# Performance work log

Measured on AMD Instinct MI355X. Metric: run time of the kernel, lower is better.

## Reference

```python
import jax, jax.numpy as jnp
import numpy as np

NUM_HEADS = 16
NEG = -1e9


def setup_inputs() -> dict:
    key = jax.random.key(0)
    ks = jax.random.split(key, 16)
    B, Sq, Skv, E = 4, 4096, 4096, 1024
    scale = 1.0 / np.sqrt(E)
    inp = {
        "q": jax.random.normal(ks[0], (B, Sq, E), jnp.float32),
        "k": jax.random.normal(ks[1], (B, Skv, E), jnp.float32),
        "v": jax.random.normal(ks[2], (B, Skv, E), jnp.float32),
        "q_padding_mask": jax.random.randint(ks[3], (B, Sq, 1), 0, 2).astype(bool),
        "key_padding_mask": jax.random.randint(ks[4], (B, Skv, 1), 0, 2).astype(bool),
        "Wq": jax.random.normal(ks[5], (E, E), jnp.float32) * scale,
        "bq": jnp.zeros((E,), jnp.float32),
        "Wk": jax.random.normal(ks[6], (E, E), jnp.float32) * scale,
        "bk": jnp.zeros((E,), jnp.float32),
        "Wv": jax.random.normal(ks[7], (E, E), jnp.float32) * scale,
        "bv": jnp.zeros((E,), jnp.float32),
        "Wp": jax.random.normal(ks[8], (E, E), jnp.float32) * scale,
        "bp": jnp.zeros((E,), jnp.float32),
    }
    return inp


def _split_heads(x, H):
    B, S, E = x.shape
    return x.reshape(B, S, H, E // H).transpose(0, 2, 1, 3)  # (B,H,S,D)


def reference(q, k, v, q_padding_mask, key_padding_mask, Wq, bq, Wk, bk, Wv, bv, Wp, bp):
    B, Sq, E = q.shape
    H = NUM_HEADS
    # padding: q*mask + ~mask*(-1e9) == where(mask, q, -1e9)
    q = jnp.where(q_padding_mask, q, NEG)
    k = jnp.where(key_padding_mask, k, NEG)
    v = v * key_padding_mask
    # projections (torch nn.Linear: x @ W.T + b)
    qh = _split_heads(q @ Wq.T + bq, H)  # (B,H,Sq,D)
    kh = _split_heads(k @ Wk.T + bk, H)  # (B,H,Skv,D)
    vh = _split_heads(v @ Wv.T + bv, H)  # (B,H,Skv,D)
    qh = jax.nn.softmax(qh, axis=-1)
    kh = jax.nn.softmax(kh, axis=-1)
    k_cumsum = kh.sum(axis=-2, keepdims=True)              # (B,H,1,D)
    a_t = 1.0 / (qh * k_cumsum).sum(axis=-1, keepdims=True)  # (B,H,Sq,1)
    context = jnp.einsum("bhsd,bhse->bhde", kh, vh)        # (B,H,D,D)
    out = jnp.einsum("bhqd,bhde->bhqe", qh, context) * a_t + qh
    out = out.transpose(0, 2, 1, 3).reshape(B, Sq, E)
    out = out @ Wp.T + bp
    return out * q_padding_mask
```

## Files before the change

### kernel.cpp

```cpp
#include <hip/hip_runtime.h>
#include <hip/hip_bf16.h>
#include <stdint.h>


typedef __bf16 bf16_t;
typedef __bf16 v8bf __attribute__((ext_vector_type(8)));
typedef __bf16 v4bf __attribute__((ext_vector_type(4)));
typedef float  v4f  __attribute__((ext_vector_type(4)));

#define NSPLIT 16

__device__ __forceinline__ void gl_lds16(const void* g, void* l) {
  __builtin_amdgcn_global_load_lds((const __attribute__((address_space(1))) void*)g,
                                   (__attribute__((address_space(3))) void*)l,
                                   16, 0, 0);
}

__global__ __launch_bounds__(256) void convert_w(
    const float* __restrict__ W0, const float* __restrict__ W1,
    const float* __restrict__ W2, const float* __restrict__ W3,
    bf16_t* __restrict__ dst)
{
  int g = blockIdx.x * 256 + threadIdx.x;
  int seg = g >> 17;
  int off = (g & 131071) * 8;
  const float* s = (seg == 0 ? W0 : seg == 1 ? W1 : seg == 2 ? W2 : W3) + off;
  v4f a = *(const v4f*)s, b = *(const v4f*)(s + 4);
  v8bf o;
#pragma unroll
  for (int j = 0; j < 4; j++) { o[j] = (bf16_t)a[j]; o[4 + j] = (bf16_t)b[j]; }
  *(v8bf*)(dst + (size_t)seg * 1048576 + off) = o;
}

__global__ __launch_bounds__(256) void convert_kv_kernel(
    const float* __restrict__ k, const float* __restrict__ v,
    bf16_t* __restrict__ kb, bf16_t* __restrict__ vb)
{
  int bid = blockIdx.x;
  const float* s; bf16_t* d;
  if (bid < 8192) { s = k; d = kb; } else { s = v; d = vb; bid -= 8192; }
  size_t i = ((size_t)bid * 256 + threadIdx.x) * 8;
  v4f a = *(const v4f*)(s + i), b = *(const v4f*)(s + i + 4);
  v8bf o;
#pragma unroll
  for (int j = 0; j < 4; j++) { o[j] = (bf16_t)a[j]; o[4 + j] = (bf16_t)b[j]; }
  *(v8bf*)(d + i) = o;
}

__global__ __launch_bounds__(256) void convert_q_kernel(
    const float* __restrict__ q, bf16_t* __restrict__ qb)
{
  size_t i = ((size_t)blockIdx.x * 256 + threadIdx.x) * 8;
  v4f a = *(const v4f*)(q + i), b = *(const v4f*)(q + i + 4);
  v8bf o;
#pragma unroll
  for (int j = 0; j < 4; j++) { o[j] = (bf16_t)a[j]; o[4 + j] = (bf16_t)b[j]; }
  *(v8bf*)(qb + i) = o;
}

__global__ __launch_bounds__(256) void rowsum_kernel(
    const float* __restrict__ Wq, const float* __restrict__ bq,
    const float* __restrict__ Wk, const float* __restrict__ bk,
    float* __restrict__ rs)
{
  int w = threadIdx.x >> 6, l = threadIdx.x & 63;
  int row = blockIdx.x * 4 + w;
  int r = (row < 1024) ? row : row - 1024;
  const float* W = ((row < 1024) ? Wq : Wk) + (size_t)r * 1024 + l * 16;
  float s = 0.f;
#pragma unroll
  for (int i = 0; i < 4; i++) {
    v4f x = *(const v4f*)(W + i * 4);
    s += x[0] + x[1] + x[2] + x[3];
  }
#pragma unroll
  for (int sh = 1; sh < 64; sh <<= 1) s += __shfl_xor(s, sh, 64);
  if (l == 0) {
    float b = (row < 1024) ? bq[r] : bk[r];
    rs[row] = -1e9f * s + b;
  }
}

template <int EPI>
__global__ __launch_bounds__(256) void gemm_bt(
    const bf16_t* __restrict__ A, const bf16_t* __restrict__ Wb,
    const float* __restrict__ bias, const int* __restrict__ rowmask,
    const float* __restrict__ rs, void* __restrict__ Cout)
{
  constexpr int K = 1024, N = 1024;
  __shared__ __align__(16) bf16_t As[2][128 * 32];
  __shared__ __align__(16) bf16_t Bs[2][128 * 32];
  const int t = threadIdx.x;
  const int l = t & 63;
  const int w = t >> 6;
  const int wm = w >> 1, wn = w & 1;
  const int xcd = blockIdx.x & 7;
  const int seq = blockIdx.x >> 3;
  const int by = ((seq >> 3) << 3) + xcd;
  const int bx = seq & 7;
  const int m0 = by << 7, n0 = bx << 7;

  const int c0 = t, c1 = t + 256;
  const bf16_t* Ag0 = A + (size_t)(m0 + (c0 >> 2)) * K + (c0 & 3) * 8;
  const bf16_t* Ag1 = A + (size_t)(m0 + (c1 >> 2)) * K + (c1 & 3) * 8;
  const bf16_t* Bg0 = Wb + (size_t)(n0 + (c0 >> 2)) * K + (c0 & 3) * 8;
  const bf16_t* Bg1 = Wb + (size_t)(n0 + (c1 >> 2)) * K + (c1 & 3) * 8;

  const int lr = l & 15;
  const int kq = (l >> 4) * 8;
  const int aOff = (wm * 64 + lr) * 32 + kq;
  const int bOff = (wn * 64 + lr) * 32 + kq;

  v4f acc[4][4] = {};

  auto stage = [&](int kt, int b) {
    gl_lds16(Ag0 + kt, &As[b][c0 * 8]);
    gl_lds16(Ag1 + kt, &As[b][c1 * 8]);
    gl_lds16(Bg0 + kt, &Bs[b][c0 * 8]);
    gl_lds16(Bg1 + kt, &Bs[b][c1 * 8]);
  };
  auto compute = [&](const bf16_t* Asb, const bf16_t* Bsb) {
    v8bf af[4], bf4[4];
#pragma unroll
    for (int r = 0; r < 4; r++) af[r] = *(const v8bf*)(Asb + aOff + r * 512);
#pragma unroll
    for (int c = 0; c < 4; c++) bf4[c] = *(const v8bf*)(Bsb + bOff + c * 512);
#pragma unroll
    for (int r = 0; r < 4; r++)
#pragma unroll
      for (int c = 0; c < 4; c++)
        acc[r][c] = __builtin_amdgcn_mfma_f32_16x16x32_bf16(af[r], bf4[c], acc[r][c], 0, 0, 0);
  };

  stage(0, 0);
  for (int kt = 0; kt < K; kt += 64) {
    __syncthreads();
    if (kt + 32 < K) stage(kt + 32, 1);
    compute(As[0], Bs[0]);
    __syncthreads();
    if (kt + 64 < K) stage(kt + 64, 0);
    compute(As[1], Bs[1]);
  }

  const int rq = (l >> 4) * 4;
  float bcol[4], rscol[4]; int colg[4];
#pragma unroll
  for (int c = 0; c < 4; c++) {
    colg[c] = n0 + wn * 64 + c * 16 + lr;
    bcol[c] = bias[colg[c]];
    rscol[c] = (EPI == 1) ? rs[colg[c]] : 0.f;
  }
#pragma unroll
  for (int r = 0; r < 4; r++) {
    int rowBase = m0 + wm * 64 + r * 16 + rq;
#pragma unroll
    for (int i = 0; i < 4; i++) {
      int row = rowBase + i;
      int msk = rowmask[row];
      float vv[4];
#pragma unroll
      for (int c = 0; c < 4; c++) {
        float x = acc[r][c][i] + bcol[c];
        if (EPI == 0)      x = msk ? x : bcol[c];
        else if (EPI == 1) x = msk ? x : rscol[c];
        else               x = msk ? x : 0.f;
        vv[c] = x;
      }
      if (EPI == 1) {
        float mx = fmaxf(fmaxf(vv[0], vv[1]), fmaxf(vv[2], vv[3]));
#pragma unroll
        for (int sh = 1; sh < 16; sh <<= 1) mx = fmaxf(mx, __shfl_xor(mx, sh, 64));
        float e0 = __expf(vv[0] - mx), e1 = __expf(vv[1] - mx);
        float e2 = __expf(vv[2] - mx), e3 = __expf(vv[3] - mx);
        float sum = e0 + e1 + e2 + e3;
#pragma unroll
        for (int sh = 1; sh < 16; sh <<= 1) sum += __shfl_xor(sum, sh, 64);
        float rinv = 1.0f / sum;
        vv[0] = e0 * rinv; vv[1] = e1 * rinv; vv[2] = e2 * rinv; vv[3] = e3 * rinv;
      }
#pragma unroll
      for (int c = 0; c < 4; c++) {
        size_t idx = (size_t)row * N + colg[c];
        if (EPI == 2) ((float*)Cout)[idx] = vv[c];
        else          ((bf16_t*)Cout)[idx] = (bf16_t)vv[c];
      }
    }
  }
}

__global__ __launch_bounds__(256) void ctx_partial(
    const bf16_t* __restrict__ kh, const bf16_t* __restrict__ vh,
    float* __restrict__ ctx, float* __restrict__ kc)
{
  __shared__ __align__(16) float khTf[2][64][36];
  __shared__ __align__(16) float vhTf[2][64][36];
  const int bh = blockIdx.x & 63;
  const int sp = blockIdx.x >> 6;
  const int b = bh >> 4, h = bh & 15;
  const int t = threadIdx.x;
  const int l = t & 63;
  const int w = t >> 6;
  const int wm = w >> 1, wn = w & 1;

  const int a  = t & 7;
  const int d0 = a * 8;
  const int sl = t >> 3;
  const int sw = sl ^ (a << 2);

  const size_t base = ((size_t)b * 4096) * 1024 + h * 64;
  const int sBeg = sp * (4096 / NSPLIT);
  const int nch = (4096 / NSPLIT) / 32;
  const bf16_t* kp = kh + base + (size_t)(sBeg + sl) * 1024 + d0;
  const bf16_t* vp = vh + base + (size_t)(sBeg + sl) * 1024 + d0;

  const int lr = l & 15;
  const int gl = l >> 4;

  v8bf ones;
#pragma unroll
  for (int j = 0; j < 8; j++) ones[j] = (bf16_t)1.0f;

  v4f acc[2][2] = {};
  v4f kca[2] = {};

  auto loadfrag = [&](const float (*T)[36], int rowbase) -> v8bf {
    const int row = rowbase + lr;
    const float* rp = &T[row][0];
    const int g0 = ((gl << 1) ^ (row >> 3)) & 7;
    v4f pa = *(const v4f*)(rp + g0 * 4);
    v4f pb = *(const v4f*)(rp + (g0 ^ 1) * 4);
    v8bf f;
#pragma unroll
    for (int j = 0; j < 4; j++) { f[j] = (bf16_t)pa[j]; f[4 + j] = (bf16_t)pb[j]; }
    return f;
  };

  v8bf rk = *(const v8bf*)kp;
  v8bf rv = *(const v8bf*)vp;
  for (int c = 0; c < nch; c++) {
    const int cur = c & 1;
#pragma unroll
    for (int j = 0; j < 8; j++) {
      khTf[cur][d0 + j][sw] = (float)rk[j];
      vhTf[cur][d0 + j][sw] = (float)rv[j];
    }
    if (c + 1 < nch) {
      rk = *(const v8bf*)(kp + (size_t)(c + 1) * 32 * 1024);
      rv = *(const v8bf*)(vp + (size_t)(c + 1) * 32 * 1024);
    }
    __syncthreads();
    v8bf af0 = loadfrag(khTf[cur], wm * 32);
    v8bf af1 = loadfrag(khTf[cur], wm * 32 + 16);
    v8bf bf0 = loadfrag(vhTf[cur], wn * 32);
    v8bf bf1 = loadfrag(vhTf[cur], wn * 32 + 16);
    acc[0][0] = __builtin_amdgcn_mfma_f32_16x16x32_bf16(af0, bf0, acc[0][0], 0, 0, 0);
    acc[0][1] = __builtin_amdgcn_mfma_f32_16x16x32_bf16(af0, bf1, acc[0][1], 0, 0, 0);
    acc[1][0] = __builtin_amdgcn_mfma_f32_16x16x32_bf16(af1, bf0, acc[1][0], 0, 0, 0);
    acc[1][1] = __builtin_amdgcn_mfma_f32_16x16x32_bf16(af1, bf1, acc[1][1], 0, 0, 0);
    if (wn == 0) {
      kca[0] = __builtin_amdgcn_mfma_f32_16x16x32_bf16(af0, ones, kca[0], 0, 0, 0);
      kca[1] = __builtin_amdgcn_mfma_f32_16x16x32_bf16(af1, ones, kca[1], 0, 0, 0);
    }
  }

  const int rq = gl * 4;
  float* cp = ctx + (size_t)bh * 4096;
#pragma unroll
  for (int r = 0; r < 2; r++)
#pragma unroll
    for (int cc = 0; cc < 2; cc++) {
      const int e = wn * 32 + cc * 16 + lr;
#pragma unroll
      for (int i = 0; i < 4; i++) {
        const int d = wm * 32 + r * 16 + rq + i;
        atomicAdd(&cp[d * 64 + e], acc[r][cc][i]);
      }
    }
  if (wn == 0 && lr == 0) {
#pragma unroll
    for (int r = 0; r < 2; r++)
#pragma unroll
      for (int i = 0; i < 4; i++) {
        const int d = wm * 32 + r * 16 + rq + i;
        atomicAdd(&kc[bh * 64 + d], kca[r][i]);
      }
  }
}

__global__ __launch_bounds__(256) void outpre_kernel(
    const bf16_t* __restrict__ qh, const float* __restrict__ ctx,
    const float* __restrict__ kc, bf16_t* __restrict__ outp)
{
  __shared__ __align__(16) bf16_t qs[128][66];
  __shared__ __align__(16) float ctxs[64][64];
  __shared__ float kcs[64];
  const int blk = blockIdx.x;
  const int st = blk & 31, h = (blk >> 5) & 15, b = blk >> 9;
  const int bh = b * 16 + h;
  const int t = threadIdx.x;
  const int s0 = st * 128;
  const size_t base = ((size_t)b * 4096 + s0) * 1024 + h * 64;

  {
    const int row = t >> 1, half = t & 1;
    const bf16_t* src = qh + base + (size_t)row * 1024 + half * 32;
#pragma unroll
    for (int j = 0; j < 4; j++) {
      v8bf qv = *(const v8bf*)(src + j * 8);
      uint32_t wv[4];
      __builtin_memcpy(wv, &qv, 16);
      uint32_t* pw = (uint32_t*)&qs[row][half * 32 + j * 8];
      pw[0] = wv[0]; pw[1] = wv[1]; pw[2] = wv[2]; pw[3] = wv[3];
    }
  }
  const float* cg = ctx + (size_t)bh * 4096;
#pragma unroll
  for (int i = 0; i < 4; i++) {
    int off = i * 1024 + t * 4;
    *(v4f*)((float*)ctxs + off) = *(const v4f*)(cg + off);
  }
  if (t < 64) kcs[t] = kc[bh * 64 + t];
  __syncthreads();

  const int er = t & 3, e0 = er * 16;
  const int rp = t >> 2;
  const int r0 = rp * 2;
  float at[2] = {};
  float acc[2][16] = {};
  for (int d = 0; d < 64; d++) {
    const float kcd = kcs[d];
    const float q0 = (float)qs[r0][d];
    const float q1 = (float)qs[r0 + 1][d];
    at[0] += q0 * kcd;
    at[1] += q1 * kcd;
    const float* cr = &ctxs[d][e0];
    v4f ca = *(const v4f*)cr,        cb = *(const v4f*)(cr + 4);
    v4f cc3 = *(const v4f*)(cr + 8), cd4 = *(const v4f*)(cr + 12);
#pragma unroll
    for (int i = 0; i < 4; i++) {
      acc[0][i]      += q0 * ca[i];   acc[1][i]      += q1 * ca[i];
      acc[0][4 + i]  += q0 * cb[i];   acc[1][4 + i]  += q1 * cb[i];
      acc[0][8 + i]  += q0 * cc3[i];  acc[1][8 + i]  += q1 * cc3[i];
      acc[0][12 + i] += q0 * cd4[i];  acc[1][12 + i] += q1 * cd4[i];
    }
  }
#pragma unroll
  for (int j = 0; j < 2; j++) {
    const int row = r0 + j;
    const float rinv = 1.0f / at[j];
    bf16_t* op = outp + base + (size_t)row * 1024 + e0;
    v8bf o0, o1;
#pragma unroll
    for (int i = 0; i < 8; i++) {
      o0[i] = (bf16_t)(acc[j][i] * rinv + (float)qs[row][e0 + i]);
      o1[i] = (bf16_t)(acc[j][8 + i] * rinv + (float)qs[row][e0 + 8 + i]);
    }
    *(v8bf*)op = o0;
    *(v8bf*)(op + 8) = o1;
  }
}

extern "C" void kernel_launch(void* const* d_in, const int* in_sizes, int n_in,
                              void* d_out, int out_size, void* d_ws, size_t ws_size,
                              hipStream_t stream)
{
  const float* q  = (const float*)d_in[0];
  const float* k  = (const float*)d_in[1];
  const float* v  = (const float*)d_in[2];
  const int* qmask = (const int*)d_in[3];
  const int* kmask = (const int*)d_in[4];
  const float* Wq = (const float*)d_in[5];
  const float* bq = (const float*)d_in[6];
  const float* Wk = (const float*)d_in[7];
  const float* bk = (const float*)d_in[8];
  const float* Wv = (const float*)d_in[9];
  const float* bv = (const float*)d_in[10];
  const float* Wp = (const float*)d_in[11];
  const float* bp = (const float*)d_in[12];

  const int M = 16384;
  char* ws = (char*)d_ws;
  size_t off = 0;
  auto alloc = [&](size_t bytes) {
    void* p = ws + off; off += (bytes + 255) & ~(size_t)255; return p;
  };
  bf16_t* wb   = (bf16_t*)alloc(4 * 1048576 * 2);
  bf16_t* abuf = (bf16_t*)alloc((size_t)M * 1024 * 2);
  float* ctx   = (float*)alloc((64 * 4096 + 64 * 64) * 4);
  float* kc    = ctx + 64 * 4096;
  float* rs    = (float*)alloc(2048 * 4);
  bf16_t* Wqb = wb, *Wkb = wb + 1048576, *Wvb = wb + 2097152, *Wpb = wb + 3145728;
  bf16_t* lo = (bf16_t*)d_out;
  bf16_t* hi = (bf16_t*)((char*)d_out + 33554432);

  hipMemsetAsync(ctx, 0, (64 * 4096 + 64 * 64) * 4, stream);
  convert_w<<<2048, 256, 0, stream>>>(Wq, Wk, Wv, Wp, wb);
  rowsum_kernel<<<512, 256, 0, stream>>>(Wq, bq, Wk, bk, rs);
  convert_kv_kernel<<<16384, 256, 0, stream>>>(k, v, lo, hi);

  const int gblocks = (M / 128) * (1024 / 128);
  gemm_bt<1><<<gblocks, 256, 0, stream>>>(lo, Wkb, bk, kmask, rs + 1024, abuf);
  gemm_bt<0><<<gblocks, 256, 0, stream>>>(hi, Wvb, bv, kmask, nullptr, lo);
  ctx_partial<<<64 * NSPLIT, 256, 0, stream>>>(abuf, lo, ctx, kc);
  convert_q_kernel<<<8192, 256, 0, stream>>>(q, hi);
  gemm_bt<1><<<gblocks, 256, 0, stream>>>(hi, Wqb, bq, qmask, rs, abuf);
  outpre_kernel<<<2048, 256, 0, stream>>>(abuf, ctx, kc, abuf);
  gemm_bt<2><<<gblocks, 256, 0, stream>>>(abuf, Wpb, bp, qmask, nullptr, d_out);
}
```

Before: 524.4 us.

## Rewrite projection GEMM with 256x256 tiles, swizzled LDS, and staggered A/B prefetch

The bf16 projection GEMM moves from 128x128 tiles with 4 waves to 256x256 tiles with 8 waves, a 64-wide K step and XOR-swizzled LDS layout to avoid bank conflicts. A and B loads are staged at different points in the loop with explicit vmcnt waits and barriers, MFMA bursts run at raised priority, and the block-to-tile mapping is remapped across XCDs. The aim is higher arithmetic intensity per LDS/global byte and better overlap of loads with MFMA. The larger tiles need 128KB LDS and many accumulators, which may limit occupancy. An extra __syncthreads is also added in the ctx_partial loop.

New measurement: 467.0 us. -10.9%, faster.

```diff
diff --git a/kernel.cpp b/kernel.cpp
--- a/kernel.cpp
+++ b/kernel.cpp
@@ -82,67 +82,116 @@
 }
 
 template <int EPI>
-__global__ __launch_bounds__(256) void gemm_bt(
+__global__ __launch_bounds__(512, 2) void gemm_bt(
     const bf16_t* __restrict__ A, const bf16_t* __restrict__ Wb,
     const float* __restrict__ bias, const int* __restrict__ rowmask,
     const float* __restrict__ rs, void* __restrict__ Cout)
 {
   constexpr int K = 1024, N = 1024;
-  __shared__ __align__(16) bf16_t As[2][128 * 32];
-  __shared__ __align__(16) bf16_t Bs[2][128 * 32];
+  constexpr int NT = 16;
+  __shared__ __align__(16) bf16_t As[2][256 * 64];
+  __shared__ __align__(16) bf16_t Bs[2][256 * 64];
   const int t = threadIdx.x;
   const int l = t & 63;
   const int w = t >> 6;
-  const int wm = w >> 1, wn = w & 1;
-  const int xcd = blockIdx.x & 7;
-  const int seq = blockIdx.x >> 3;
-  const int by = ((seq >> 3) << 3) + xcd;
-  const int bx = seq & 7;
-  const int m0 = by << 7, n0 = bx << 7;
-
-  const int c0 = t, c1 = t + 256;
-  const bf16_t* Ag0 = A + (size_t)(m0 + (c0 >> 2)) * K + (c0 & 3) * 8;
-  const bf16_t* Ag1 = A + (size_t)(m0 + (c1 >> 2)) * K + (c1 & 3) * 8;
-  const bf16_t* Bg0 = Wb + (size_t)(n0 + (c0 >> 2)) * K + (c0 & 3) * 8;
-  const bf16_t* Bg1 = Wb + (size_t)(n0 + (c1 >> 2)) * K + (c1 & 3) * 8;
-
-  const int lr = l & 15;
-  const int kq = (l >> 4) * 8;
-  const int aOff = (wm * 64 + lr) * 32 + kq;
-  const int bOff = (wn * 64 + lr) * 32 + kq;
-
-  v4f acc[4][4] = {};
-
-  auto stage = [&](int kt, int b) {
-    gl_lds16(Ag0 + kt, &As[b][c0 * 8]);
-    gl_lds16(Ag1 + kt, &As[b][c1 * 8]);
-    gl_lds16(Bg0 + kt, &Bs[b][c0 * 8]);
-    gl_lds16(Bg1 + kt, &Bs[b][c1 * 8]);
+  const int wm = w >> 2, wn = w & 3;
+  const int g  = (blockIdx.x & 7) * 32 + (blockIdx.x >> 3);
+  const int by = g & 63, bx = g >> 6;
+  const int m0 = by << 8, n0 = bx << 8;
+
+  const int srow = t >> 3;
+  const int sgs  = (t & 7) ^ (srow & 7);
+  const bf16_t* Ag = A  + (size_t)(m0 + srow) * K + sgs * 8;
+  const bf16_t* Bg = Wb + (size_t)(n0 + srow) * K + sgs * 8;
+  bf16_t* lA = &As[0][0] + t * 8;
+  bf16_t* lB = &Bs[0][0] + t * 8;
+
+  auto stageA = [&](int half, int kt, int buf) {
+    const bf16_t* s = Ag + (size_t)(half * 128) * K + (kt << 6);
+    bf16_t* d = lA + buf * 16384 + half * 8192;
+    gl_lds16(s, d);
+    gl_lds16(s + (size_t)64 * K, d + 4096);
   };
-  auto compute = [&](const bf16_t* Asb, const bf16_t* Bsb) {
-    v8bf af[4], bf4[4];
-#pragma unroll
-    for (int r = 0; r < 4; r++) af[r] = *(const v8bf*)(Asb + aOff + r * 512);
-#pragma unroll
-    for (int c = 0; c < 4; c++) bf4[c] = *(const v8bf*)(Bsb + bOff + c * 512);
-#pragma unroll
-    for (int r = 0; r < 4; r++)
-#pragma unroll
-      for (int c = 0; c < 4; c++)
-        acc[r][c] = __builtin_amdgcn_mfma_f32_16x16x32_bf16(af[r], bf4[c], acc[r][c], 0, 0, 0);
+  auto stageB = [&](int half, int kt, int buf) {
+    const bf16_t* s = Bg + (size_t)(half * 128) * K + (kt << 6);
+    bf16_t* d = lB + buf * 16384 + half * 8192;
+    gl_lds16(s, d);
+    gl_lds16(s + (size_t)64 * K, d + 4096);
   };
 
-  stage(0, 0);
-  for (int kt = 0; kt < K; kt += 64) {
-    __syncthreads();
-    if (kt + 32 < K) stage(kt + 32, 1);
-    compute(As[0], Bs[0]);
-    __syncthreads();
-    if (kt + 64 < K) stage(kt + 64, 0);
-    compute(As[1], Bs[1]);
-  }
-
-  const int rq = (l >> 4) * 4;
+  const int lr = l & 15, kg = l >> 4;
+  const int xg0 = ((kg)     ^ (lr & 7)) * 8;
+  const int xg1 = ((4 + kg) ^ (lr & 7)) * 8;
+  const int aB = (wm * 128 + lr) * 64;
+  const int bB = (wn * 64  + lr) * 64;
+
+  v4f acc[8][4] = {};
+  v8bf bfr[4][2];
+
+#define QUAD(R0, R1, A0_, A1_, A2_, A3_)                                        \
+  {                                                                             \
+    __builtin_amdgcn_s_setprio(1);                                              \
+    _Pragma("unroll")                                                           \
+    for (int c = 0; c < 4; ++c) {                                               \
+      acc[R0][c] = __builtin_amdgcn_mfma_f32_16x16x32_bf16(A0_, bfr[c][0], acc[R0][c], 0, 0, 0); \
+      acc[R0][c] = __builtin_amdgcn_mfma_f32_16x16x32_bf16(A1_, bfr[c][1], acc[R0][c], 0, 0, 0); \
+      acc[R1][c] = __builtin_amdgcn_mfma_f32_16x16x32_bf16(A2_, bfr[c][0], acc[R1][c], 0, 0, 0); \
+      acc[R1][c] = __builtin_amdgcn_mfma_f32_16x16x32_bf16(A3_, bfr[c][1], acc[R1][c], 0, 0, 0); \
+    }                                                                           \
+    __builtin_amdgcn_s_setprio(0);                                              \
+  }
+
+  stageA(0, 0, 0); stageA(1, 0, 0); stageB(0, 0, 0); stageB(1, 0, 0);
+  stageB(0, 1, 1); stageB(1, 1, 1);
+  asm volatile("s_waitcnt vmcnt(4)" ::: "memory");
+  __builtin_amdgcn_s_barrier();
+
+  for (int s = 0; s < NT; ++s) {
+    const int b = s & 1;
+    const bf16_t* Ab = &As[b][0];
+    const bf16_t* Bb = &Bs[b][0];
+    v8bf a0, a1, a2, a3;
+#pragma unroll
+    for (int c = 0; c < 4; ++c) {
+      bfr[c][0] = *(const v8bf*)(Bb + bB + c * 1024 + xg0);
+      bfr[c][1] = *(const v8bf*)(Bb + bB + c * 1024 + xg1);
+    }
+    a0 = *(const v8bf*)(Ab + aB + 0 * 1024 + xg0);
+    a1 = *(const v8bf*)(Ab + aB + 0 * 1024 + xg1);
+    a2 = *(const v8bf*)(Ab + aB + 1 * 1024 + xg0);
+    a3 = *(const v8bf*)(Ab + aB + 1 * 1024 + xg1);
+    if (s + 1 < NT) { stageA(0, s + 1, b ^ 1); stageA(1, s + 1, b ^ 1); }
+    __builtin_amdgcn_s_barrier();
+    QUAD(0, 1, a0, a1, a2, a3);
+    __builtin_amdgcn_s_barrier();
+    a0 = *(const v8bf*)(Ab + aB + 2 * 1024 + xg0);
+    a1 = *(const v8bf*)(Ab + aB + 2 * 1024 + xg1);
+    a2 = *(const v8bf*)(Ab + aB + 3 * 1024 + xg0);
+    a3 = *(const v8bf*)(Ab + aB + 3 * 1024 + xg1);
+    __builtin_amdgcn_s_barrier();
+    QUAD(2, 3, a0, a1, a2, a3);
+    __builtin_amdgcn_s_barrier();
+    a0 = *(const v8bf*)(Ab + aB + 4 * 1024 + xg0);
+    a1 = *(const v8bf*)(Ab + aB + 4 * 1024 + xg1);
+    a2 = *(const v8bf*)(Ab + aB + 5 * 1024 + xg0);
+    a3 = *(const v8bf*)(Ab + aB + 5 * 1024 + xg1);
+    if (s + 2 < NT) { stageB(0, s + 2, b); stageB(1, s + 2, b); }
+    __builtin_amdgcn_s_barrier();
+    QUAD(4, 5, a0, a1, a2, a3);
+    __builtin_amdgcn_s_barrier();
+    a0 = *(const v8bf*)(Ab + aB + 6 * 1024 + xg0);
+    a1 = *(const v8bf*)(Ab + aB + 6 * 1024 + xg1);
+    a2 = *(const v8bf*)(Ab + aB + 7 * 1024 + xg0);
+    a3 = *(const v8bf*)(Ab + aB + 7 * 1024 + xg1);
+    __builtin_amdgcn_s_barrier();
+    QUAD(6, 7, a0, a1, a2, a3);
+    if (s < NT - 2) asm volatile("s_waitcnt vmcnt(4)" ::: "memory");
+    else            asm volatile("s_waitcnt vmcnt(0)" ::: "memory");
+    __builtin_amdgcn_s_barrier();
+  }
+#undef QUAD
+
+  const int rq = kg * 4;
   float bcol[4], rscol[4]; int colg[4];
 #pragma unroll
   for (int c = 0; c < 4; c++) {
@@ -151,8 +200,8 @@
     rscol[c] = (EPI == 1) ? rs[colg[c]] : 0.f;
   }
 #pragma unroll
-  for (int r = 0; r < 4; r++) {
-    int rowBase = m0 + wm * 64 + r * 16 + rq;
+  for (int r = 0; r < 8; r++) {
+    int rowBase = m0 + wm * 128 + r * 16 + rq;
 #pragma unroll
     for (int i = 0; i < 4; i++) {
       int row = rowBase + i;
@@ -261,6 +310,7 @@
       kca[0] = __builtin_amdgcn_mfma_f32_16x16x32_bf16(af0, ones, kca[0], 0, 0, 0);
       kca[1] = __builtin_amdgcn_mfma_f32_16x16x32_bf16(af1, ones, kca[1], 0, 0, 0);
     }
+    __syncthreads();
   }
 
   const int rq = gl * 4;
@@ -398,12 +448,12 @@
   rowsum_kernel<<<512, 256, 0, stream>>>(Wq, bq, Wk, bk, rs);
   convert_kv_kernel<<<16384, 256, 0, stream>>>(k, v, lo, hi);
 
-  const int gblocks = (M / 128) * (1024 / 128);
-  gemm_bt<1><<<gblocks, 256, 0, stream>>>(lo, Wkb, bk, kmask, rs + 1024, abuf);
-  gemm_bt<0><<<gblocks, 256, 0, stream>>>(hi, Wvb, bv, kmask, nullptr, lo);
+  const int gblocks = (M / 256) * (1024 / 256);
+  gemm_bt<1><<<gblocks, 512, 0, stream>>>(lo, Wkb, bk, kmask, rs + 1024, abuf);
+  gemm_bt<0><<<gblocks, 512, 0, stream>>>(hi, Wvb, bv, kmask, nullptr, lo);
   ctx_partial<<<64 * NSPLIT, 256, 0, stream>>>(abuf, lo, ctx, kc);
   convert_q_kernel<<<8192, 256, 0, stream>>>(q, hi);
-  gemm_bt<1><<<gblocks, 256, 0, stream>>>(hi, Wqb, bq, qmask, rs, abuf);
+  gemm_bt<1><<<gblocks, 512, 0, stream>>>(hi, Wqb, bq, qmask, rs, abuf);
   outpre_kernel<<<2048, 256, 0, stream>>>(abuf, ctx, kc, abuf);
-  gemm_bt<2><<<gblocks, 256, 0, stream>>>(abuf, Wpb, bp, qmask, nullptr, d_out);
-}
+  gemm_bt<2><<<gblocks, 512, 0, stream>>>(abuf, Wpb, bp, qmask, nullptr, d_out);
+}
```
